# Performance work log

Hardware: AMD Instinct MI355X
Metric: run time of the kernel (lower is better)

## Reference

```python
import jax, jax.numpy as jnp
import numpy as np

# Module-level constants (chosen values, see shape_source)
NB = 24      # num_blocks (hardcoded in DualArmActionHead)
D = 512      # hidden_dim
H = 8        # num_heads (block default)
HD = D // H  # head_dim = 64
NTT = 64     # num_task_tokens
NPA = 8      # NUM_TOKENS_PER_ARM
NAC = 8      # NUM_ACTIONS_CHUNK (query length T)
B = 8        # batch
L_DIM = 7    # LEFT_ARM_DIM
R_DIM = 7    # RIGHT_ARM_DIM

# Per-block linear order inside the (NB, 11, D, D) weight stacks:
# 0:q 1:k_self 2:v_self 3:k_task 4:v_task 5:k_adap 6:v_adap 7:k_inter 8:v_inter 9:o 10:ffn

def _rope_tables(T):
    inv_freq = 1.0 / (10000.0 ** (jnp.arange(0, HD, 2, dtype=jnp.float32) / HD))
    t = jnp.arange(T, dtype=jnp.float32)
    freqs = jnp.einsum('i,j->ij', t, inv_freq)            # (T, HD/2)
    emb = jnp.concatenate([freqs, freqs], axis=-1)        # (T, HD)
    return jnp.cos(emb), jnp.sin(emb)

def _rotate_half(x):
    x1 = x[..., ::2]
    x2 = x[..., 1::2]
    return jnp.stack((-x2, x1), axis=-1).reshape(x.shape)

def _apply_rope(q, k, cos, sin):
    cos = cos[None, None]
    sin = sin[None, None]
    return q * cos + _rotate_half(q) * sin, k * cos + _rotate_half(k) * sin

def _ln(x, g, b):
    mu = jnp.mean(x, axis=-1, keepdims=True)
    var = jnp.var(x, axis=-1, keepdims=True)
    return (x - mu) / jnp.sqrt(var + 1e-5) * g + b

def _mh(t):  # (B, L, D) -> (B, H, L, HD)
    b, l, _ = t.shape
    return t.reshape(b, l, H, HD).transpose(0, 2, 1, 3)

def _arm(xq, x_other, h_t, h_a, W, b, lng, lnb, g, cos, sin):
    def lin(i, inp):
        return inp @ W[i] + b[i]
    q = _mh(lin(0, xq))
    ks, vs = _mh(lin(1, xq)), _mh(lin(2, xq))
    kt, vt = _mh(lin(3, h_t)), _mh(lin(4, h_t))
    ka, va = _mh(lin(5, h_a)), _mh(lin(6, h_a))
    ki, vi = _mh(lin(7, x_other)), _mh(lin(8, x_other))
    q, ks = _apply_rope(q, ks, cos, sin)
    _, ki = _apply_rope(ki, ki, cos, sin)
    scores = jnp.concatenate([
        jnp.einsum('bhqd,bhkd->bhqk', q, ks),
        jnp.einsum('bhqd,bhkd->bhqk', q, ka),
        g * jnp.einsum('bhqd,bhkd->bhqk', q, kt),
        jnp.einsum('bhqd,bhkd->bhqk', q, ki),
    ], axis=-1) / np.sqrt(HD).astype(np.float32)
    attn = jax.nn.softmax(scores, axis=-1)
    vals = jnp.concatenate([vs, va, vt, vi], axis=2)      # (B,H,Ktot,HD)
    out = jnp.einsum('bhqk,bhkd->bhqd', attn, vals)
    out = out.transpose(0, 2, 1, 3).reshape(xq.shape)
    out = out @ W[9] + b[9]
    y = out + xq
    return jax.nn.relu(_ln(y, lng, lnb) @ W[10] + b[10])


def setup_inputs() -> dict:
    key = jax.random.key(0)
    ks = jax.random.split(key, 8)
    ahs = jax.random.normal(ks[0], (B, NB + 1, NTT + 2 * NPA, D), dtype=jnp.float32)
    W_L = 0.02 * jax.random.normal(ks[1], (NB, 11, D, D), dtype=jnp.float32)
    W_R = 0.02 * jax.random.normal(ks[2], (NB, 11, D, D), dtype=jnp.float32)
    b_L = jnp.zeros((NB, 11, D), jnp.float32)
    b_R = jnp.zeros((NB, 11, D), jnp.float32)
    lng_L = jnp.ones((NB, D), jnp.float32)
    lnb_L = jnp.zeros((NB, D), jnp.float32)
    lng_R = jnp.ones((NB, D), jnp.float32)
    lnb_R = jnp.zeros((NB, D), jnp.float32)
    gating = 0.1 * jax.random.normal(ks[3], (NB,), dtype=jnp.float32)
    fln_g_L = jnp.ones((D,), jnp.float32)
    fln_b_L = jnp.zeros((D,), jnp.float32)
    fln_g_R = jnp.ones((D,), jnp.float32)
    fln_b_R = jnp.zeros((D,), jnp.float32)
    fc_W_L = 0.02 * jax.random.normal(ks[4], (D, L_DIM), dtype=jnp.float32)
    fc_b_L = jnp.zeros((L_DIM,), jnp.float32)
    fc_W_R = 0.02 * jax.random.normal(ks[5], (D, R_DIM), dtype=jnp.float32)
    fc_b_R = jnp.zeros((R_DIM,), jnp.float32)
    return dict(actions_hidden_states=ahs, W_L=W_L, b_L=b_L, lng_L=lng_L, lnb_L=lnb_L,
                W_R=W_R, b_R=b_R, lng_R=lng_R, lnb_R=lnb_R, gating=gating,
                fln_g_L=fln_g_L, fln_b_L=fln_b_L, fln_g_R=fln_g_R, fln_b_R=fln_b_R,
                fc_W_L=fc_W_L, fc_b_L=fc_b_L, fc_W_R=fc_W_R, fc_b_R=fc_b_R)


def reference(actions_hidden_states, W_L, b_L, lng_L, lnb_L, W_R, b_R, lng_R, lnb_R,
              gating, fln_g_L, fln_b_L, fln_g_R, fln_b_R, fc_W_L, fc_b_L, fc_W_R, fc_b_R):
    ahs = actions_hidden_states
    # per-layer conditioning tokens: layer i uses index i+1 along dim 1
    h_t = jnp.swapaxes(ahs[:, 1:NB + 1, :NTT, :], 0, 1)                 # (NB,B,NTT,D)
    h_aL = jnp.swapaxes(ahs[:, 1:NB + 1, NTT:NTT + NPA, :], 0, 1)       # (NB,B,NPA,D)
    h_aR = jnp.swapaxes(ahs[:, 1:NB + 1, NTT + NPA:, :], 0, 1)          # (NB,B,NPA,D)
    cos, sin = _rope_tables(NAC)
    x0 = jnp.zeros((ahs.shape[0], NAC, D), ahs.dtype)

    def step(carry, xs):
        xL, xR = carry
        wL, bl, gL, bbL, wR, br, gR, bbR, gt, ht, haL, haR = xs
        g = jnp.tanh(gt)
        nL = _arm(xL, xR, ht, haL, wL, bl, gL, bbL, g, cos, sin)
        nR = _arm(xR, xL, ht, haR, wR, br, gR, bbR, g, cos, sin)
        return (nL, nR), None

    (xL, xR), _ = jax.lax.scan(step, (x0, x0),
                               (W_L, b_L, lng_L, lnb_L, W_R, b_R, lng_R, lnb_R,
                                gating, h_t, h_aL, h_aR))
    outL = _ln(xL, fln_g_L, fln_b_L) @ fc_W_L + fc_b_L
    outR = _ln(xR, fln_g_R, fln_b_R) @ fc_W_R + fc_b_R
    return jnp.concatenate([outL, outR], axis=-1)   # (B, NAC, 14)
```

## Files before the change

kernel.cpp:

```cpp
#include <hip/hip_runtime.h>

#define DD 512
#define NBLK 24

typedef short s16x8 __attribute__((ext_vector_type(8)));
typedef float f32x4 __attribute__((ext_vector_type(4)));

union FragU { s16x8 s; __bf16 h[8]; };

__device__ __forceinline__ f32x4 mfma16(s16x8 a, s16x8 b, f32x4 c) {
  return __builtin_amdgcn_mfma_f32_16x16x32_bf16(a, b, c, 0, 0, 0);
}

__device__ __forceinline__ void bsplit(float v, __bf16& hi, __bf16& lo) {
  hi = (__bf16)v;
  lo = (__bf16)(v - (float)hi);
}

template<int AMODE, bool RESID>
__device__ __forceinline__ void gemm64_core(
    const float* __restrict__ Abase, int rshift, long sOuter,
    const float* __restrict__ Wf,
    const float* __restrict__ bias,
    const float* __restrict__ lng, const float* __restrict__ lnb,
    const float* __restrict__ resid,
    float* __restrict__ outF,
    int n0)
{
  const int tid  = threadIdx.x;
  const int wave = tid >> 6;
  const int lane = tid & 63;
  const int l15  = lane & 15;
  const int lq   = lane >> 4;

  const int rowA = wave * 16 + l15;
  const float* Arow = Abase + (long)(rowA >> rshift) * sOuter
                            + (long)(rowA & ((1 << rshift) - 1)) * DD;

  float mu = 0.f, rstd = 0.f;
  if constexpr (AMODE == 2) {
    float s = 0.f, ss = 0.f;
    const float* p = Arow + lq * 128;
    #pragma unroll
    for (int k = 0; k < 128; k += 4) {
      float4 v = *reinterpret_cast<const float4*>(p + k);
      s  += v.x + v.y + v.z + v.w;
      ss += v.x * v.x + v.y * v.y + v.z * v.z + v.w * v.w;
    }
    s += __shfl_xor(s, 16); ss += __shfl_xor(ss, 16);
    s += __shfl_xor(s, 32); ss += __shfl_xor(ss, 32);
    mu = s * (1.f / 512.f);
    float var = ss * (1.f / 512.f) - mu * mu;
    rstd = rsqrtf(var + 1e-5f);
  }

  f32x4 acc[4] = {};

  for (int ks = 0; ks < 16; ++ks) {
    const int k0 = ks * 32 + lq * 8;
    FragU ahi, alo;
    {
      float4 v0 = *reinterpret_cast<const float4*>(Arow + k0);
      float4 v1 = *reinterpret_cast<const float4*>(Arow + k0 + 4);
      float t0[8] = {v0.x, v0.y, v0.z, v0.w, v1.x, v1.y, v1.z, v1.w};
      if constexpr (AMODE == 2) {
        float4 g0 = *reinterpret_cast<const float4*>(lng + k0);
        float4 g1 = *reinterpret_cast<const float4*>(lng + k0 + 4);
        float4 c0 = *reinterpret_cast<const float4*>(lnb + k0);
        float4 c1 = *reinterpret_cast<const float4*>(lnb + k0 + 4);
        float gg[8] = {g0.x, g0.y, g0.z, g0.w, g1.x, g1.y, g1.z, g1.w};
        float cc[8] = {c0.x, c0.y, c0.z, c0.w, c1.x, c1.y, c1.z, c1.w};
        #pragma unroll
        for (int e = 0; e < 8; ++e) {
          float v = (t0[e] - mu) * rstd * gg[e] + cc[e];
          bsplit(v, ahi.h[e], alo.h[e]);
        }
      } else {
        #pragma unroll
        for (int e = 0; e < 8; ++e) {
          float v = t0[e];
          if constexpr (AMODE == 1) v = fmaxf(v, 0.f);
          bsplit(v, ahi.h[e], alo.h[e]);
        }
      }
    }
    const float* wp = Wf + (long)k0 * DD + n0 + l15;
    #pragma unroll
    for (int j = 0; j < 4; ++j) {
      FragU bhi, blo;
      #pragma unroll
      for (int e = 0; e < 8; ++e) {
        float w = wp[(long)e * DD + j * 16];
        bsplit(w, bhi.h[e], blo.h[e]);
      }
      acc[j] = mfma16(ahi.s, bhi.s, acc[j]);
      acc[j] = mfma16(ahi.s, blo.s, acc[j]);
      acc[j] = mfma16(alo.s, bhi.s, acc[j]);
    }
  }

  const int mbase = wave * 16 + lq * 4;
  #pragma unroll
  for (int j = 0; j < 4; ++j) {
    const int n = n0 + j * 16 + l15;
    const float bv = bias[n];
    #pragma unroll
    for (int r = 0; r < 4; ++r) {
      const int m = mbase + r;
      float v = acc[j][r] + bv;
      if constexpr (RESID) v += fmaxf(resid[(long)m * DD + n], 0.f);
      outF[(long)m * DD + n] = v;
    }
  }
}

#define LDSW 40

__global__ __launch_bounds__(256) void k_p1t(
    const float* __restrict__ ahs,
    const float* __restrict__ WL, const float* __restrict__ WR,
    const float* __restrict__ bL, const float* __restrict__ bR,
    float* __restrict__ kvt)
{
  __shared__ __align__(16) unsigned short Ab[2][64 * LDSW];
  __shared__ __align__(16) unsigned short Wb[4][2][64 * LDSW];

  const int bx = blockIdx.x;
  const int ntile = bx & 7, mtile = (bx >> 3) & 7, nb = bx >> 6;
  const int n0 = ntile * 64;

  const float* Abase = ahs + (long)(mtile * 25 + nb + 1) * 80 * DD;
  const float* Wp[4];
  const float* bp[4];
  #pragma unroll
  for (int o = 0; o < 4; ++o) {
    const int arm = o >> 1, kv = o & 1;
    Wp[o] = (arm ? WR : WL) + (long)(nb * 11 + 3 + kv) * DD * DD;
    bp[o] = (arm ? bR : bL) + (long)(nb * 11 + 3 + kv) * DD;
  }

  const int tid  = threadIdx.x;
  const int srow = tid >> 2;
  const int skq  = (tid & 3) * 8;
  const int wave = tid >> 6, lane = tid & 63, l15 = lane & 15, lq = lane >> 4;

  f32x4 acc[4][4] = {};
  float aR[8];
  float wRg[4][8];

  auto loadStage = [&](int kbase) {
    const float* ap = Abase + (long)srow * DD + kbase + skq;
    float4 v0 = *reinterpret_cast<const float4*>(ap);
    float4 v1 = *reinterpret_cast<const float4*>(ap + 4);
    aR[0] = v0.x; aR[1] = v0.y; aR[2] = v0.z; aR[3] = v0.w;
    aR[4] = v1.x; aR[5] = v1.y; aR[6] = v1.z; aR[7] = v1.w;
    #pragma unroll
    for (int o = 0; o < 4; ++o) {
      #pragma unroll
      for (int e = 0; e < 8; ++e)
        wRg[o][e] = Wp[o][(long)(kbase + skq + e) * DD + n0 + srow];
    }
  };

  loadStage(0);
  for (int s = 0; s < 16; ++s) {
    __syncthreads();
    {
      FragU uh, ul;
      #pragma unroll
      for (int e = 0; e < 8; ++e) bsplit(aR[e], uh.h[e], ul.h[e]);
      *reinterpret_cast<s16x8*>(&Ab[0][srow * LDSW + skq]) = uh.s;
      *reinterpret_cast<s16x8*>(&Ab[1][srow * LDSW + skq]) = ul.s;
      #pragma unroll
      for (int o = 0; o < 4; ++o) {
        FragU wh, wl;
        #pragma unroll
        for (int e = 0; e < 8; ++e) bsplit(wRg[o][e], wh.h[e], wl.h[e]);
        *reinterpret_cast<s16x8*>(&Wb[o][0][srow * LDSW + skq]) = wh.s;
        *reinterpret_cast<s16x8*>(&Wb[o][1][srow * LDSW + skq]) = wl.s;
      }
    }
    __syncthreads();
    if (s < 15) loadStage((s + 1) * 32);
    s16x8 ahi = *reinterpret_cast<const s16x8*>(&Ab[0][(wave * 16 + l15) * LDSW + lq * 8]);
    s16x8 alo = *reinterpret_cast<const s16x8*>(&Ab[1][(wave * 16 + l15) * LDSW + lq * 8]);
    #pragma unroll
    for (int o = 0; o < 4; ++o) {
      #pragma unroll
      for (int j = 0; j < 4; ++j) {
        s16x8 bhi = *reinterpret_cast<const s16x8*>(&Wb[o][0][(j * 16 + l15) * LDSW + lq * 8]);
        s16x8 blo = *reinterpret_cast<const s16x8*>(&Wb[o][1][(j * 16 + l15) * LDSW + lq * 8]);
        acc[o][j] = mfma16(ahi, bhi, acc[o][j]);
        acc[o][j] = mfma16(ahi, blo, acc[o][j]);
        acc[o][j] = mfma16(alo, bhi, acc[o][j]);
      }
    }
  }

  const int mbase = mtile * 64 + wave * 16 + lq * 4;
  #pragma unroll
  for (int o = 0; o < 4; ++o) {
    float* outb = kvt + (long)(nb * 4 + o) * 512 * DD;
    #pragma unroll
    for (int j = 0; j < 4; ++j) {
      const int n = n0 + j * 16 + l15;
      const float bv = bp[o][n];
      #pragma unroll
      for (int r = 0; r < 4; ++r)
        outb[(long)(mbase + r) * DD + n] = acc[o][j][r] + bv;
    }
  }
}

__global__ __launch_bounds__(256) void k_p1a(
    const float* __restrict__ ahs,
    const float* __restrict__ WL, const float* __restrict__ WR,
    const float* __restrict__ bL, const float* __restrict__ bR,
    float* __restrict__ kva)
{
  const int bx = blockIdx.x;
  const int ntile = bx & 7, kv = (bx >> 3) & 1, arm = (bx >> 4) & 1, nb = bx >> 5;
  const float* Abase = ahs + ((long)(nb + 1) * 80 + 64 + arm * 8) * DD;
  const float* W    = (arm ? WR : WL) + (long)(nb * 11 + 5 + kv) * DD * DD;
  const float* bias = (arm ? bR : bL) + (long)(nb * 11 + 5 + kv) * DD;
  float* out = kva + (long)(nb * 4 + arm * 2 + kv) * 64 * DD;
  gemm64_core<0, false>(Abase, 3, (long)25 * 80 * DD, W, bias,
                        nullptr, nullptr, nullptr, out, ntile * 64);
}

__global__ __launch_bounds__(256) void k_qkv(
    const float* __restrict__ x,
    const float* __restrict__ WL, const float* __restrict__ WR,
    const float* __restrict__ bL, const float* __restrict__ bR,
    float* __restrict__ qkv, int nb)
{
  const int bx = blockIdx.x;
  const int arm = bx / 40;
  const int rem = bx - arm * 40;
  const int wi = rem >> 3, ntile = rem & 7;
  const int w = (wi < 3) ? wi : wi + 4;
  const float* A    = x + (long)((wi < 3) ? arm : (1 - arm)) * 64 * DD;
  const float* W    = (arm ? WR : WL) + (long)(nb * 11 + w) * DD * DD;
  const float* bias = (arm ? bR : bL) + (long)(nb * 11 + w) * DD;
  float* out = qkv + (long)(arm * 5 + wi) * 64 * DD;
  gemm64_core<1, false>(A, 6, 0, W, bias, nullptr, nullptr, nullptr,
                        out, ntile * 64);
}

__global__ __launch_bounds__(512) void k_attn(
    const float* __restrict__ qkv, const float* __restrict__ kvt,
    const float* __restrict__ kva, const float* __restrict__ gating,
    const float* __restrict__ ropeC, const float* __restrict__ ropeS,
    float* __restrict__ attnout, int nb)
{
  __shared__ float kb[88 * 65];
  __shared__ float vb[88 * 65];
  __shared__ float qb[8 * 65];
  __shared__ float pb[8 * 89];

  const int bx = blockIdx.x;
  const int h = bx & 7, b = (bx >> 3) & 7, arm = bx >> 6;
  const int tid = threadIdx.x;
  const float g = tanhf(gating[nb]);

  {
    const int p = tid >> 6, d = tid & 63;
    const float* qrow = qkv + ((long)(arm * 5 + 0) * 64 + b * 8 + p) * DD + h * 64;
    float v = qrow[d], vp = qrow[d ^ 1];
    float c = ropeC[p * 64 + d], s = ropeS[p * 64 + d];
    qb[p * 65 + d] = v * c + ((d & 1) ? vp : -vp) * s;
  }
  for (int idx = tid; idx < 88 * 64; idx += 512) {
    const int j = idx >> 6, d = idx & 63;
    float kvval, vvval;
    if (j < 8) {
      const float* krow = qkv + ((long)(arm * 5 + 1) * 64 + b * 8 + j) * DD + h * 64;
      float v = krow[d], vp = krow[d ^ 1];
      float c = ropeC[j * 64 + d], s = ropeS[j * 64 + d];
      kvval = v * c + ((d & 1) ? vp : -vp) * s;
      vvval = qkv[((long)(arm * 5 + 2) * 64 + b * 8 + j) * DD + h * 64 + d];
    } else if (j < 16) {
      const int t = j - 8;
      kvval = kva[((long)(nb * 4 + arm * 2 + 0) * 64 + b * 8 + t) * DD + h * 64 + d];
      vvval = kva[((long)(nb * 4 + arm * 2 + 1) * 64 + b * 8 + t) * DD + h * 64 + d];
    } else if (j < 80) {
      const int t = j - 16;
      kvval = g * kvt[((long)(nb * 4 + arm * 2 + 0) * 512 + b * 64 + t) * DD + h * 64 + d];
      vvval = kvt[((long)(nb * 4 + arm * 2 + 1) * 512 + b * 64 + t) * DD + h * 64 + d];
    } else {
      const int t = j - 80;
      const float* krow = qkv + ((long)(arm * 5 + 3) * 64 + b * 8 + t) * DD + h * 64;
      float v = krow[d], vp = krow[d ^ 1];
      float c = ropeC[t * 64 + d], s = ropeS[t * 64 + d];
      kvval = v * c + ((d & 1) ? vp : -vp) * s;
      vvval = qkv[((long)(arm * 5 + 4) * 64 + b * 8 + t) * DD + h * 64 + d];
    }
    kb[j * 65 + d] = kvval;
    vb[j * 65 + d] = vvval;
  }
  __syncthreads();

  const int p = tid >> 6, lane = tid & 63;
  float s0 = 0.f, s1 = 0.f;
  const int j2 = 64 + ((lane < 24) ? lane : 0);
  #pragma unroll 8
  for (int d = 0; d < 64; ++d) {
    const float q = qb[p * 65 + d];
    s0 += q * kb[lane * 65 + d];
    s1 += q * kb[j2 * 65 + d];
  }
  s0 *= 0.125f; s1 *= 0.125f;
  float m = (lane < 24) ? fmaxf(s0, s1) : s0;
  #pragma unroll
  for (int off = 1; off < 64; off <<= 1) m = fmaxf(m, __shfl_xor(m, off));
  const float e0 = __expf(s0 - m);
  const float e1 = (lane < 24) ? __expf(s1 - m) : 0.f;
  float sum = e0 + e1;
  #pragma unroll
  for (int off = 1; off < 64; off <<= 1) sum += __shfl_xor(sum, off);
  const float inv = 1.f / sum;
  pb[p * 89 + lane] = e0 * inv;
  if (lane < 24) pb[p * 89 + 64 + lane] = e1 * inv;
  __syncthreads();

  float acc = 0.f;
  #pragma unroll 8
  for (int j = 0; j < 88; ++j) acc += pb[p * 89 + j] * vb[j * 65 + lane];
  attnout[((long)arm * 64 + b * 8 + p) * DD + h * 64 + lane] = acc;
}

__global__ __launch_bounds__(256) void k_proj(
    const float* __restrict__ attnout,
    const float* __restrict__ WL, const float* __restrict__ WR,
    const float* __restrict__ bL, const float* __restrict__ bR,
    const float* __restrict__ x, float* __restrict__ y, int nb)
{
  const int bx = blockIdx.x;
  const int arm = bx >> 3, ntile = bx & 7;
  const float* A    = attnout + (long)arm * 64 * DD;
  const float* W    = (arm ? WR : WL) + (long)(nb * 11 + 9) * DD * DD;
  const float* bias = (arm ? bR : bL) + (long)(nb * 11 + 9) * DD;
  gemm64_core<0, true>(A, 6, 0, W, bias, nullptr, nullptr,
                       x + (long)arm * 64 * DD,
                       y + (long)arm * 64 * DD, ntile * 64);
}

__global__ __launch_bounds__(256) void k_ffn(
    const float* __restrict__ y,
    const float* __restrict__ WL, const float* __restrict__ WR,
    const float* __restrict__ bL, const float* __restrict__ bR,
    const float* __restrict__ lngL, const float* __restrict__ lnbL,
    const float* __restrict__ lngR, const float* __restrict__ lnbR,
    float* __restrict__ x, int nb)
{
  const int bx = blockIdx.x;
  const int arm = bx >> 3, ntile = bx & 7;
  const float* A    = y + (long)arm * 64 * DD;
  const float* W    = (arm ? WR : WL) + (long)(nb * 11 + 10) * DD * DD;
  const float* bias = (arm ? bR : bL) + (long)(nb * 11 + 10) * DD;
  const float* g    = (arm ? lngR : lngL) + (long)nb * DD;
  const float* bb   = (arm ? lnbR : lnbL) + (long)nb * DD;
  gemm64_core<2, false>(A, 6, 0, W, bias, g, bb, nullptr,
                        x + (long)arm * 64 * DD, ntile * 64);
}

__global__ __launch_bounds__(64) void k_final(
    const float* __restrict__ x,
    const float* __restrict__ fgL, const float* __restrict__ fbL,
    const float* __restrict__ fgR, const float* __restrict__ fbR,
    const float* __restrict__ fwL, const float* __restrict__ fcbL,
    const float* __restrict__ fwR, const float* __restrict__ fcbR,
    float* __restrict__ out)
{
  const int bx = blockIdx.x;
  const int b = bx & 7, arm = bx >> 3;
  const int tid = threadIdx.x;
  const int p = tid >> 3, k8 = tid & 7;
  const float* xr = x + ((long)arm * 64 + b * 8 + p) * DD;

  float s = 0.f, ss = 0.f;
  for (int k = k8 * 64; k < k8 * 64 + 64; k += 4) {
    float4 v = *reinterpret_cast<const float4*>(xr + k);
    float a0 = fmaxf(v.x, 0.f), a1 = fmaxf(v.y, 0.f);
    float a2 = fmaxf(v.z, 0.f), a3 = fmaxf(v.w, 0.f);
    s  += a0 + a1 + a2 + a3;
    ss += a0 * a0 + a1 * a1 + a2 * a2 + a3 * a3;
  }
  s += __shfl_xor(s, 1); ss += __shfl_xor(ss, 1);
  s += __shfl_xor(s, 2); ss += __shfl_xor(ss, 2);
  s += __shfl_xor(s, 4); ss += __shfl_xor(ss, 4);
  const float mu = s * (1.f / 512.f);
  const float var = ss * (1.f / 512.f) - mu * mu;
  const float rstd = rsqrtf(var + 1e-5f);

  const float* g   = arm ? fgR : fgL;
  const float* bb  = arm ? fbR : fbL;
  const float* fw  = arm ? fwR : fwL;
  const float* fcb = arm ? fcbR : fcbL;
  const int j = k8;
  if (j < 7) {
    float acc = 0.f;
    for (int k = 0; k < 512; ++k) {
      const float xn = (fmaxf(xr[k], 0.f) - mu) * rstd * g[k] + bb[k];
      acc += xn * fw[k * 7 + j];
    }
    out[((long)(b * 8) + p) * 14 + arm * 7 + j] = acc + fcb[j];
  }
}

__global__ void k_init(float* __restrict__ x, float* __restrict__ ropeC,
                       float* __restrict__ ropeS)
{
  const int t = blockIdx.x * 256 + threadIdx.x;
  if (t < 2 * 64 * DD) x[t] = 0.f;
  if (t < 512) {
    const int p = t >> 6, d = t & 63;
    const float inv = expf(-(float)(d & 31) * (9.210340371976184f / 32.f));
    const float ang = (float)p * inv;
    ropeC[t] = cosf(ang);
    ropeS[t] = sinf(ang);
  }
}

extern "C" void kernel_launch(void* const* d_in, const int* in_sizes, int n_in,
                              void* d_out, int out_size, void* d_ws, size_t ws_size,
                              hipStream_t stream)
{
  (void)in_sizes; (void)n_in; (void)out_size; (void)ws_size;

  const float* ahs  = (const float*)d_in[0];
  const float* WL   = (const float*)d_in[1];
  const float* bL   = (const float*)d_in[2];
  const float* lngL = (const float*)d_in[3];
  const float* lnbL = (const float*)d_in[4];
  const float* WR   = (const float*)d_in[5];
  const float* bR   = (const float*)d_in[6];
  const float* lngR = (const float*)d_in[7];
  const float* lnbR = (const float*)d_in[8];
  const float* gating = (const float*)d_in[9];
  const float* fgL  = (const float*)d_in[10];
  const float* fbL  = (const float*)d_in[11];
  const float* fgR  = (const float*)d_in[12];
  const float* fbR  = (const float*)d_in[13];
  const float* fwL  = (const float*)d_in[14];
  const float* fcbL = (const float*)d_in[15];
  const float* fwR  = (const float*)d_in[16];
  const float* fcbR = (const float*)d_in[17];
  float* out = (float*)d_out;

  char* ws = (char*)d_ws;
  size_t off = 0;
  float* ropeC = (float*)(ws + off); off += 512 * 4;
  float* ropeS = (float*)(ws + off); off += 512 * 4;
  float* x     = (float*)(ws + off); off += (size_t)2 * 64 * DD * 4;
  float* qkv   = (float*)(ws + off); off += (size_t)2 * 5 * 64 * DD * 4;
  float* attno = (float*)(ws + off); off += (size_t)2 * 64 * DD * 4;
  float* y     = (float*)(ws + off); off += (size_t)2 * 64 * DD * 4;
  float* kvt   = (float*)(ws + off); off += (size_t)NBLK * 4 * 512 * DD * 4;
  float* kva   = (float*)(ws + off); off += (size_t)NBLK * 4 * 64 * DD * 4;

  k_init<<<dim3(256), dim3(256), 0, stream>>>(x, ropeC, ropeS);
  k_p1t <<<dim3(1536), dim3(256), 0, stream>>>(ahs, WL, WR, bL, bR, kvt);
  k_p1a <<<dim3(768),  dim3(256), 0, stream>>>(ahs, WL, WR, bL, bR, kva);

  for (int nb = 0; nb < NBLK; ++nb) {
    k_qkv <<<dim3(80),  dim3(256), 0, stream>>>(x, WL, WR, bL, bR, qkv, nb);
    k_attn<<<dim3(128), dim3(512), 0, stream>>>(qkv, kvt, kva, gating, ropeC, ropeS, attno, nb);
    k_proj<<<dim3(16),  dim3(256), 0, stream>>>(attno, WL, WR, bL, bR, x, y, nb);
    k_ffn <<<dim3(16),  dim3(256), 0, stream>>>(y, WL, WR, bL, bR, lngL, lnbL, lngR, lnbR, x, nb);
  }
  k_final<<<dim3(16), dim3(64), 0, stream>>>(x, fgL, fbL, fgR, fbR, fwL, fcbL, fwR, fcbR, out);
}
```

Before: 1.952 ms.

## Prepack weights into bf16 MFMA layout and split per-layer GEMMs across more blocks

A new pre-pass kernel converts the per-layer q/k/v, interaction k/v, output and FFN weights into a hi/lo bf16 split stored in MFMA fragment order. The per-layer QKV, projection and FFN kernels switch to a 16-column-tile GEMM with far more blocks. The projection and FFN GEMMs are split along K into two partial buffers, and the next consumer (including LayerNorm and the final head) sums those partials. The goal is better use of the GPU on the latency-bound serial chain of small launches, in exchange for a large up-front weight conversion pass and extra workspace. The new path runs only when the workspace is large enough; otherwise the old kernels are used.

```diff
diff --git a/kernel.cpp b/kernel.cpp
--- a/kernel.cpp
+++ b/kernel.cpp
@@ -2,6 +2,8 @@
 
 #define DD 512
 #define NBLK 24
+#define BLK (64 * DD)
+#define WT_SLOT 524288
 
 typedef short s16x8 __attribute__((ext_vector_type(8)));
 typedef float f32x4 __attribute__((ext_vector_type(4)));
@@ -15,6 +17,9 @@
 __device__ __forceinline__ void bsplit(float v, __bf16& hi, __bf16& lo) {
   hi = (__bf16)v;
   lo = (__bf16)(v - (float)hi);
+}
+__device__ __forceinline__ unsigned short f2hi(float v) {
+  union { __bf16 h; unsigned short u; } cv; cv.h = (__bf16)v; return cv.u;
 }
 
 template<int AMODE, bool RESID>
@@ -114,6 +119,150 @@
   }
 }
 
+template<int AMODE, bool A2P>
+__device__ __forceinline__ void gemm16t(
+    const float* __restrict__ A1, const float* __restrict__ A2,
+    const unsigned short* __restrict__ Wt,
+    const float* __restrict__ bias, int addBias,
+    const float* __restrict__ lng, const float* __restrict__ lnb,
+    const float* __restrict__ r1, const float* __restrict__ r2,
+    float* __restrict__ outF, int n0, int ks0, int ks1)
+{
+  const int tid  = threadIdx.x;
+  const int wave = tid >> 6;
+  const int lane = tid & 63;
+  const int l15  = lane & 15;
+  const int lq   = lane >> 4;
+
+  const int rowA = wave * 16 + l15;
+  const float* A1row = A1 + (long)rowA * DD;
+  const float* A2row = A2P ? (A2 + (long)rowA * DD) : nullptr;
+
+  float mu = 0.f, rstd = 0.f;
+  if constexpr (AMODE == 2) {
+    float s = 0.f, ss = 0.f;
+    const float* p1 = A1row + lq * 128;
+    const float* p2 = A2P ? (A2row + lq * 128) : nullptr;
+    #pragma unroll
+    for (int k = 0; k < 128; k += 4) {
+      float4 v = *reinterpret_cast<const float4*>(p1 + k);
+      float vx = v.x, vy = v.y, vz = v.z, vw = v.w;
+      if constexpr (A2P) {
+        float4 u = *reinterpret_cast<const float4*>(p2 + k);
+        vx += u.x; vy += u.y; vz += u.z; vw += u.w;
+      }
+      s  += vx + vy + vz + vw;
+      ss += vx * vx + vy * vy + vz * vz + vw * vw;
+    }
+    s += __shfl_xor(s, 16); ss += __shfl_xor(ss, 16);
+    s += __shfl_xor(s, 32); ss += __shfl_xor(ss, 32);
+    mu = s * (1.f / 512.f);
+    float var = ss * (1.f / 512.f) - mu * mu;
+    rstd = rsqrtf(var + 1e-5f);
+  }
+
+  f32x4 acc = {};
+  const long ngBase = (long)(n0 >> 4) * 64;
+
+  for (int ks = ks0; ks < ks1; ++ks) {
+    const int k0 = ks * 32 + lq * 8;
+    FragU ahi, alo;
+    {
+      float4 v0 = *reinterpret_cast<const float4*>(A1row + k0);
+      float4 v1 = *reinterpret_cast<const float4*>(A1row + k0 + 4);
+      float t0[8] = {v0.x, v0.y, v0.z, v0.w, v1.x, v1.y, v1.z, v1.w};
+      if constexpr (A2P) {
+        float4 u0 = *reinterpret_cast<const float4*>(A2row + k0);
+        float4 u1 = *reinterpret_cast<const float4*>(A2row + k0 + 4);
+        t0[0] += u0.x; t0[1] += u0.y; t0[2] += u0.z; t0[3] += u0.w;
+        t0[4] += u1.x; t0[5] += u1.y; t0[6] += u1.z; t0[7] += u1.w;
+      }
+      if constexpr (AMODE == 2) {
+        float4 g0 = *reinterpret_cast<const float4*>(lng + k0);
+        float4 g1 = *reinterpret_cast<const float4*>(lng + k0 + 4);
+        float4 c0 = *reinterpret_cast<const float4*>(lnb + k0);
+        float4 c1 = *reinterpret_cast<const float4*>(lnb + k0 + 4);
+        float gg[8] = {g0.x, g0.y, g0.z, g0.w, g1.x, g1.y, g1.z, g1.w};
+        float cc[8] = {c0.x, c0.y, c0.z, c0.w, c1.x, c1.y, c1.z, c1.w};
+        #pragma unroll
+        for (int e = 0; e < 8; ++e) {
+          float v = (t0[e] - mu) * rstd * gg[e] + cc[e];
+          bsplit(v, ahi.h[e], alo.h[e]);
+        }
+      } else {
+        #pragma unroll
+        for (int e = 0; e < 8; ++e) {
+          float v = t0[e];
+          if constexpr (AMODE == 1) v = fmaxf(v, 0.f);
+          bsplit(v, ahi.h[e], alo.h[e]);
+        }
+      }
+    }
+    const unsigned short* wp = Wt + ((ngBase + (ks * 4 + lq)) * 16 + l15) * 16;
+    s16x8 bhi = *reinterpret_cast<const s16x8*>(wp);
+    s16x8 blo = *reinterpret_cast<const s16x8*>(wp + 8);
+    acc = mfma16(ahi.s, bhi, acc);
+    acc = mfma16(ahi.s, blo, acc);
+    acc = mfma16(alo.s, bhi, acc);
+  }
+
+  const int mbase = wave * 16 + lq * 4;
+  const int n = n0 + l15;
+  const float bv = addBias ? bias[n] : 0.f;
+  #pragma unroll
+  for (int r = 0; r < 4; ++r) {
+    const int m = mbase + r;
+    float v = acc[r] + bv;
+    if (r1) {
+      float rv = r1[(long)m * DD + n];
+      if (r2) rv += r2[(long)m * DD + n];
+      v += fmaxf(rv, 0.f);
+    }
+    outF[(long)m * DD + n] = v;
+  }
+}
+
+__constant__ int c_wmap[7] = {0, 1, 2, 7, 8, 9, 10};
+
+__global__ __launch_bounds__(256) void k_wt(
+    const float* __restrict__ WL, const float* __restrict__ WR,
+    unsigned short* __restrict__ Wt)
+{
+  const int bx = blockIdx.x;
+  const int ng = bx & 31, slot = bx >> 5;
+  const int wi7 = slot % 7, nb2 = slot / 7;
+  const int arm = nb2 & 1, nb = nb2 >> 1;
+  const float* Wsrc = (arm ? WR : WL) + (long)(nb * 11 + c_wmap[wi7]) * DD * DD;
+
+  const int t = threadIdx.x;
+  const int k8 = t >> 2, lbase = (t & 3) * 4;
+
+  unsigned short hi[4][8], lo[4][8];
+  #pragma unroll
+  for (int e = 0; e < 8; ++e) {
+    float4 v = *reinterpret_cast<const float4*>(
+        Wsrc + (long)(k8 * 8 + e) * DD + ng * 16 + lbase);
+    float vv[4] = {v.x, v.y, v.z, v.w};
+    #pragma unroll
+    for (int c = 0; c < 4; ++c) {
+      __bf16 h, l;
+      bsplit(vv[c], h, l);
+      union { __bf16 b; unsigned short u; } ch, cl; ch.b = h; cl.b = l;
+      hi[c][e] = ch.u; lo[c][e] = cl.u;
+    }
+  }
+  unsigned short* dst = Wt + (long)slot * WT_SLOT
+                      + ((long)(ng * 64 + k8) * 16 + lbase) * 16;
+  #pragma unroll
+  for (int c = 0; c < 4; ++c) {
+    s16x8 a, b;
+    #pragma unroll
+    for (int e = 0; e < 8; ++e) { ((short*)&a)[e] = hi[c][e]; ((short*)&b)[e] = lo[c][e]; }
+    *reinterpret_cast<s16x8*>(dst + c * 16)     = a;
+    *reinterpret_cast<s16x8*>(dst + c * 16 + 8) = b;
+  }
+}
+
 #define LDSW 40
 
 __global__ __launch_bounds__(256) void k_p1t(
@@ -228,7 +377,70 @@
                         nullptr, nullptr, nullptr, out, ntile * 64);
 }
 
-__global__ __launch_bounds__(256) void k_qkv(
+__global__ __launch_bounds__(256) void k_qkvT(
+    const float* __restrict__ xp, const unsigned short* __restrict__ Wt,
+    const float* __restrict__ bL, const float* __restrict__ bR,
+    float* __restrict__ qkv, int nb)
+{
+  const int bx = blockIdx.x;
+  const int arm = bx / 160;
+  const int rem = bx - arm * 160;
+  const int wi = rem >> 5, ntile = rem & 31;
+  const int sel = (wi < 3) ? arm : (1 - arm);
+  const float* A1 = xp + (long)sel * BLK;
+  const float* A2 = xp + (long)(2 + sel) * BLK;
+  const long slot = ((long)nb * 2 + arm) * 7 + wi;
+  const unsigned short* W = Wt + slot * WT_SLOT;
+  const float* bias = (arm ? bR : bL) + (long)(nb * 11 + c_wmap[wi]) * DD;
+  float* out = qkv + (long)(arm * 5 + wi) * BLK;
+  gemm16t<1, true>(A1, A2, W, bias, 1, nullptr, nullptr, nullptr, nullptr,
+                   out, ntile * 16, 0, 16);
+}
+
+__global__ __launch_bounds__(256) void k_projT(
+    const float* __restrict__ attno, const unsigned short* __restrict__ Wt,
+    const float* __restrict__ bL, const float* __restrict__ bR,
+    const float* __restrict__ xp, float* __restrict__ yp, int nb)
+{
+  const int bx = blockIdx.x;
+  const int arm = bx >> 6;
+  const int rem = bx & 63;
+  const int kh = rem >> 5, ntile = rem & 31;
+  const long slot = ((long)nb * 2 + arm) * 7 + 5;
+  const unsigned short* W = Wt + slot * WT_SLOT;
+  const float* bias = (arm ? bR : bL) + (long)(nb * 11 + 9) * DD;
+  const float* A1 = attno + (long)arm * BLK;
+  const float* r1 = (kh == 0) ? xp + (long)arm * BLK : nullptr;
+  const float* r2 = (kh == 0) ? xp + (long)(2 + arm) * BLK : nullptr;
+  float* out = yp + (long)(kh * 2 + arm) * BLK;
+  gemm16t<0, false>(A1, nullptr, W, bias, kh == 0, nullptr, nullptr, r1, r2,
+                    out, ntile * 16, kh * 8, kh * 8 + 8);
+}
+
+__global__ __launch_bounds__(256) void k_ffnT(
+    const float* __restrict__ yp, const unsigned short* __restrict__ Wt,
+    const float* __restrict__ bL, const float* __restrict__ bR,
+    const float* __restrict__ lngL, const float* __restrict__ lnbL,
+    const float* __restrict__ lngR, const float* __restrict__ lnbR,
+    float* __restrict__ xp, int nb)
+{
+  const int bx = blockIdx.x;
+  const int arm = bx >> 6;
+  const int rem = bx & 63;
+  const int kh = rem >> 5, ntile = rem & 31;
+  const long slot = ((long)nb * 2 + arm) * 7 + 6;
+  const unsigned short* W = Wt + slot * WT_SLOT;
+  const float* bias = (arm ? bR : bL) + (long)(nb * 11 + 10) * DD;
+  const float* g  = (arm ? lngR : lngL) + (long)nb * DD;
+  const float* bb = (arm ? lnbR : lnbL) + (long)nb * DD;
+  const float* A1 = yp + (long)arm * BLK;
+  const float* A2 = yp + (long)(2 + arm) * BLK;
+  float* out = xp + (long)(kh * 2 + arm) * BLK;
+  gemm16t<2, true>(A1, A2, W, bias, kh == 0, g, bb, nullptr, nullptr,
+                   out, ntile * 16, kh * 8, kh * 8 + 8);
+}
+
+__global__ __launch_bounds__(256) void k_qkv_g(
     const float* __restrict__ x,
     const float* __restrict__ WL, const float* __restrict__ WR,
     const float* __restrict__ bL, const float* __restrict__ bR,
@@ -239,12 +451,46 @@
   const int rem = bx - arm * 40;
   const int wi = rem >> 3, ntile = rem & 7;
   const int w = (wi < 3) ? wi : wi + 4;
-  const float* A    = x + (long)((wi < 3) ? arm : (1 - arm)) * 64 * DD;
+  const float* A    = x + (long)((wi < 3) ? arm : (1 - arm)) * BLK;
   const float* W    = (arm ? WR : WL) + (long)(nb * 11 + w) * DD * DD;
   const float* bias = (arm ? bR : bL) + (long)(nb * 11 + w) * DD;
-  float* out = qkv + (long)(arm * 5 + wi) * 64 * DD;
+  float* out = qkv + (long)(arm * 5 + wi) * BLK;
   gemm64_core<1, false>(A, 6, 0, W, bias, nullptr, nullptr, nullptr,
                         out, ntile * 64);
+}
+
+__global__ __launch_bounds__(256) void k_proj_g(
+    const float* __restrict__ attno,
+    const float* __restrict__ WL, const float* __restrict__ WR,
+    const float* __restrict__ bL, const float* __restrict__ bR,
+    const float* __restrict__ x, float* __restrict__ y, int nb)
+{
+  const int bx = blockIdx.x;
+  const int arm = bx >> 3, ntile = bx & 7;
+  const float* A    = attno + (long)arm * BLK;
+  const float* W    = (arm ? WR : WL) + (long)(nb * 11 + 9) * DD * DD;
+  const float* bias = (arm ? bR : bL) + (long)(nb * 11 + 9) * DD;
+  gemm64_core<0, true>(A, 6, 0, W, bias, nullptr, nullptr,
+                       x + (long)arm * BLK, y + (long)arm * BLK, ntile * 64);
+}
+
+__global__ __launch_bounds__(256) void k_ffn_g(
+    const float* __restrict__ y,
+    const float* __restrict__ WL, const float* __restrict__ WR,
+    const float* __restrict__ bL, const float* __restrict__ bR,
+    const float* __restrict__ lngL, const float* __restrict__ lnbL,
+    const float* __restrict__ lngR, const float* __restrict__ lnbR,
+    float* __restrict__ x, int nb)
+{
+  const int bx = blockIdx.x;
+  const int arm = bx >> 3, ntile = bx & 7;
+  const float* A    = y + (long)arm * BLK;
+  const float* W    = (arm ? WR : WL) + (long)(nb * 11 + 10) * DD * DD;
+  const float* bias = (arm ? bR : bL) + (long)(nb * 11 + 10) * DD;
+  const float* g    = (arm ? lngR : lngL) + (long)nb * DD;
+  const float* bb   = (arm ? lnbR : lnbL) + (long)nb * DD;
+  gemm64_core<2, false>(A, 6, 0, W, bias, g, bb, nullptr,
+                        x + (long)arm * BLK, ntile * 64);
 }
 
 __global__ __launch_bounds__(512) void k_attn(
@@ -329,43 +575,8 @@
   attnout[((long)arm * 64 + b * 8 + p) * DD + h * 64 + lane] = acc;
 }
 
-__global__ __launch_bounds__(256) void k_proj(
-    const float* __restrict__ attnout,
-    const float* __restrict__ WL, const float* __restrict__ WR,
-    const float* __restrict__ bL, const float* __restrict__ bR,
-    const float* __restrict__ x, float* __restrict__ y, int nb)
-{
-  const int bx = blockIdx.x;
-  const int arm = bx >> 3, ntile = bx & 7;
-  const float* A    = attnout + (long)arm * 64 * DD;
-  const float* W    = (arm ? WR : WL) + (long)(nb * 11 + 9) * DD * DD;
-  const float* bias = (arm ? bR : bL) + (long)(nb * 11 + 9) * DD;
-  gemm64_core<0, true>(A, 6, 0, W, bias, nullptr, nullptr,
-                       x + (long)arm * 64 * DD,
-                       y + (long)arm * 64 * DD, ntile * 64);
-}
-
-__global__ __launch_bounds__(256) void k_ffn(
-    const float* __restrict__ y,
-    const float* __restrict__ WL, const float* __restrict__ WR,
-    const float* __restrict__ bL, const float* __restrict__ bR,
-    const float* __restrict__ lngL, const float* __restrict__ lnbL,
-    const float* __restrict__ lngR, const float* __restrict__ lnbR,
-    float* __restrict__ x, int nb)
-{
-  const int bx = blockIdx.x;
-  const int arm = bx >> 3, ntile = bx & 7;
-  const float* A    = y + (long)arm * 64 * DD;
-  const float* W    = (arm ? WR : WL) + (long)(nb * 11 + 10) * DD * DD;
-  const float* bias = (arm ? bR : bL) + (long)(nb * 11 + 10) * DD;
-  const float* g    = (arm ? lngR : lngL) + (long)nb * DD;
-  const float* bb   = (arm ? lnbR : lnbL) + (long)nb * DD;
-  gemm64_core<2, false>(A, 6, 0, W, bias, g, bb, nullptr,
-                        x + (long)arm * 64 * DD, ntile * 64);
-}
-
 __global__ __launch_bounds__(64) void k_final(
-    const float* __restrict__ x,
+    const float* __restrict__ xp,
     const float* __restrict__ fgL, const float* __restrict__ fbL,
     const float* __restrict__ fgR, const float* __restrict__ fbR,
     const float* __restrict__ fwL, const float* __restrict__ fcbL,
@@ -376,13 +587,15 @@
   const int b = bx & 7, arm = bx >> 3;
   const int tid = threadIdx.x;
   const int p = tid >> 3, k8 = tid & 7;
-  const float* xr = x + ((long)arm * 64 + b * 8 + p) * DD;
+  const float* xr1 = xp + ((long)arm * 64 + b * 8 + p) * DD;
+  const float* xr2 = xr1 + 2 * BLK;
 
   float s = 0.f, ss = 0.f;
   for (int k = k8 * 64; k < k8 * 64 + 64; k += 4) {
-    float4 v = *reinterpret_cast<const float4*>(xr + k);
-    float a0 = fmaxf(v.x, 0.f), a1 = fmaxf(v.y, 0.f);
-    float a2 = fmaxf(v.z, 0.f), a3 = fmaxf(v.w, 0.f);
+    float4 v = *reinterpret_cast<const float4*>(xr1 + k);
+    float4 u = *reinterpret_cast<const float4*>(xr2 + k);
+    float a0 = fmaxf(v.x + u.x, 0.f), a1 = fmaxf(v.y + u.y, 0.f);
+    float a2 = fmaxf(v.z + u.z, 0.f), a3 = fmaxf(v.w + u.w, 0.f);
     s  += a0 + a1 + a2 + a3;
     ss += a0 * a0 + a1 * a1 + a2 * a2 + a3 * a3;
   }
@@ -401,18 +614,19 @@
   if (j < 7) {
     float acc = 0.f;
     for (int k = 0; k < 512; ++k) {
-      const float xn = (fmaxf(xr[k], 0.f) - mu) * rstd * g[k] + bb[k];
+      const float xv = fmaxf(xr1[k] + xr2[k], 0.f);
+      const float xn = (xv - mu) * rstd * g[k] + bb[k];
       acc += xn * fw[k * 7 + j];
     }
     out[((long)(b * 8) + p) * 14 + arm * 7 + j] = acc + fcb[j];
   }
 }
 
-__global__ void k_init(float* __restrict__ x, float* __restrict__ ropeC,
+__global__ void k_init(float* __restrict__ xp, float* __restrict__ ropeC,
                        float* __restrict__ ropeS)
 {
   const int t = blockIdx.x * 256 + threadIdx.x;
-  if (t < 2 * 64 * DD) x[t] = 0.f;
+  if (t < 4 * BLK) xp[t] = 0.f;
   if (t < 512) {
     const int p = t >> 6, d = t & 63;
     const float inv = expf(-(float)(d & 31) * (9.210340371976184f / 32.f));
@@ -426,7 +640,7 @@
                               void* d_out, int out_size, void* d_ws, size_t ws_size,
                               hipStream_t stream)
 {
-  (void)in_sizes; (void)n_in; (void)out_size; (void)ws_size;
+  (void)in_sizes; (void)n_in; (void)out_size;
 
   const float* ahs  = (const float*)d_in[0];
   const float* WL   = (const float*)d_in[1];
@@ -452,22 +666,35 @@
   size_t off = 0;
   float* ropeC = (float*)(ws + off); off += 512 * 4;
   float* ropeS = (float*)(ws + off); off += 512 * 4;
-  float* x     = (float*)(ws + off); off += (size_t)2 * 64 * DD * 4;
-  float* qkv   = (float*)(ws + off); off += (size_t)2 * 5 * 64 * DD * 4;
-  float* attno = (float*)(ws + off); off += (size_t)2 * 64 * DD * 4;
-  float* y     = (float*)(ws + off); off += (size_t)2 * 64 * DD * 4;
+  float* xp    = (float*)(ws + off); off += (size_t)4 * BLK * 4;
+  float* qkv   = (float*)(ws + off); off += (size_t)10 * BLK * 4;
+  float* attno = (float*)(ws + off); off += (size_t)2 * BLK * 4;
+  float* yp    = (float*)(ws + off); off += (size_t)4 * BLK * 4;
   float* kvt   = (float*)(ws + off); off += (size_t)NBLK * 4 * 512 * DD * 4;
   float* kva   = (float*)(ws + off); off += (size_t)NBLK * 4 * 64 * DD * 4;
-
-  k_init<<<dim3(256), dim3(256), 0, stream>>>(x, ropeC, ropeS);
+  unsigned short* Wt = (unsigned short*)(ws + off);
+  const size_t need = off + (size_t)NBLK * 2 * 7 * WT_SLOT * 2;
+
+  const bool useT = (ws_size >= need);
+
+  k_init<<<dim3(512), dim3(256), 0, stream>>>(xp, ropeC, ropeS);
+  if (useT)
+    k_wt<<<dim3(336 * 32), dim3(256), 0, stream>>>(WL, WR, Wt);
   k_p1t <<<dim3(1536), dim3(256), 0, stream>>>(ahs, WL, WR, bL, bR, kvt);
   k_p1a <<<dim3(768),  dim3(256), 0, stream>>>(ahs, WL, WR, bL, bR, kva);
 
   for (int nb = 0; nb < NBLK; ++nb) {
-    k_qkv <<<dim3(80),  dim3(256), 0, stream>>>(x, WL, WR, bL, bR, qkv, nb);
-    k_attn<<<dim3(128), dim3(512), 0, stream>>>(qkv, kvt, kva, gating, ropeC, ropeS, attno, nb);
-    k_proj<<<dim3(16),  dim3(256), 0, stream>>>(attno, WL, WR, bL, bR, x, y, nb);
-    k_ffn <<<dim3(16),  dim3(256), 0, stream>>>(y, WL, WR, bL, bR, lngL, lnbL, lngR, lnbR, x, nb);
-  }
-  k_final<<<dim3(16), dim3(64), 0, stream>>>(x, fgL, fbL, fgR, fbR, fwL, fcbL, fwR, fcbR, out);
-}
+    if (useT) {
+      k_qkvT<<<dim3(320), dim3(256), 0, stream>>>(xp, Wt, bL, bR, qkv, nb);
+      k_attn<<<dim3(128), dim3(512), 0, stream>>>(qkv, kvt, kva, gating, ropeC, ropeS, attno, nb);
+      k_projT<<<dim3(128), dim3(256), 0, stream>>>(attno, Wt, bL, bR, xp, yp, nb);
+      k_ffnT<<<dim3(128), dim3(256), 0, stream>>>(yp, Wt, bL, bR, lngL, lnbL, lngR, lnbR, xp, nb);
+    } else {
+      k_qkv_g<<<dim3(80),  dim3(256), 0, stream>>>(xp, WL, WR, bL, bR, qkv, nb);
+      k_attn<<<dim3(128), dim3(512), 0, stream>>>(qkv, kvt, kva, gating, ropeC, ropeS, attno, nb);
+      k_proj_g<<<dim3(16),  dim3(256), 0, stream>>>(attno, WL, WR, bL, bR, xp, yp, nb);
+      k_ffn_g<<<dim3(16),  dim3(256), 0, stream>>>(yp, WL, WR, bL, bR, lngL, lnbL, lngR, lnbR, xp, nb);
+    }
+  }
+  k_final<<<dim3(16), dim3(64), 0, stream>>>(xp, fgL, fbL, fgR, fbR, fwL, fcbL, fwR, fcbR, out);
+}
```

Result: faster. 1.858 ms (-4.8%).
